# Optimization experiments

Measured on AMD Instinct MI355X. Metric: run time of the kernel, lower is better.

Reference implementation:

```python
import jax, jax.numpy as jnp
import numpy as np

_SAMPLING_EPS = 1e-5
BIG_NEG = jnp.float32(-1e30)  # finite stand-in for -inf (exact 0 after softmax in fp32)


def setup_inputs() -> dict:
    key = jax.random.key(0)
    ks = jax.random.split(key, 12)
    B, V, P, O, S = 128, 128000, 2048, 256, 4
    return {
        "logits": jax.random.normal(ks[0], (B, V), jnp.float32) * 4.0,
        "prompt_token_ids": jax.random.randint(ks[1], (B, P), 0, V),
        "output_token_ids": jax.random.randint(ks[2], (B, O), 0, V),
        "stop_token_ids": jax.random.randint(ks[3], (B, S), 0, V),
        "min_tokens": jax.random.randint(ks[4], (B,), 0, 512),
        "presence_penalties": jax.random.uniform(ks[5], (B,), jnp.float32),
        "frequency_penalties": jax.random.uniform(ks[6], (B,), jnp.float32),
        "repetition_penalties": 1.0 + 0.3 * jax.random.uniform(ks[7], (B,), jnp.float32),
        "temperature": 0.5 + jax.random.uniform(ks[8], (B,), jnp.float32),
        "top_k": jax.random.randint(ks[9], (B,), 32, 64),
        "top_p": 0.5 + 0.5 * jax.random.uniform(ks[10], (B,), jnp.float32),
        "uniform_noise": jax.random.uniform(ks[11], (B, V), jnp.float32, minval=1e-10, maxval=1.0),
        "max_num_logprobs": 20,
    }


def reference(logits, prompt_token_ids, output_token_ids, stop_token_ids,
              min_tokens, presence_penalties, frequency_penalties,
              repetition_penalties, temperature, top_k, top_p,
              uniform_noise, max_num_logprobs):
    B, V = logits.shape
    x = logits.astype(jnp.float32)
    rows = jnp.arange(B)[:, None]

    # ---- min-token penalty: set stop-token logits to -inf while len(output) < min_tokens
    need = min_tokens > output_token_ids.shape[1]                  # [B]
    stop_pen = jnp.where(need[:, None], BIG_NEG, jnp.inf)          # [B,S]
    x = x.at[rows, stop_token_ids].min(stop_pen)

    # ---- presence / frequency / repetition penalties (vLLM apply_penalties)
    counts = jnp.zeros((B, V), jnp.float32).at[rows, output_token_ids].add(1.0)
    prompt_mask = jnp.zeros((B, V), bool).at[rows, prompt_token_ids].set(True)
    output_mask = counts > 0
    rp = repetition_penalties[:, None]
    penalized = jnp.where(x > 0, x / rp, x * rp)
    x = jnp.where(prompt_mask | output_mask, penalized, x)
    x = x - frequency_penalties[:, None] * counts \
          - presence_penalties[:, None] * output_mask.astype(jnp.float32)

    # ---- temperature (greedy rows: temp treated as 1.0)
    t = jnp.where(temperature < _SAMPLING_EPS, 1.0, temperature)
    x = x / t[:, None]

    # ---- top-k / top-p filtering (per-row k and p)
    order = jnp.argsort(-x, axis=-1)                               # descending
    srt = jnp.take_along_axis(x, order, axis=-1)
    pos = jnp.arange(V)[None, :]
    k_eff = jnp.where(top_k < 1, V, top_k)
    keep_k = pos < k_eff[:, None]
    probs_s = jax.nn.softmax(srt, axis=-1)
    cum = jnp.cumsum(probs_s, axis=-1)
    keep_p = (cum - probs_s) < top_p[:, None]                      # cumulative mass before token < p
    keep = jnp.zeros((B, V), bool).at[rows, order].set(keep_k & keep_p)
    x = jnp.where(keep, x, BIG_NEG)

    orig_logits = x
    # source applies temperature a second time before the final sample
    x2 = x / t[:, None]

    # ---- sample: Gumbel-max random sampling, greedy where temperature ~ 0
    gumbel = -jnp.log(-jnp.log(uniform_noise))
    random_sampled = jnp.argmax(x2 + gumbel, axis=-1)
    greedy_sampled = jnp.argmax(x2, axis=-1)
    sampled = jnp.where(temperature < _SAMPLING_EPS, greedy_sampled,
                        random_sampled).astype(jnp.int32)

    # ---- top-k logprobs
    logprobs = jax.nn.log_softmax(orig_logits, axis=-1)
    topk_logprobs, topk_indices = jax.lax.top_k(logprobs, max_num_logprobs)
    return sampled, topk_logprobs, topk_indices.astype(jnp.int32)
```

## Files before the change

kernel.cpp:

```cpp
#include <hip/hip_runtime.h>
#include <math.h>

#define VV 128000
#define NB 128
#define PP 2048
#define OO 256

#define S   8
#define CH  16000
#define CW  500
#define NT1 256
#define CAP 128
#define HS1 512

#define NT2 256
#define MC  (S*CAP)

#define BIG_NEG_F (-1e30f)
#define PAD_KEY 0x007FFFFF80000000ULL
#define LOG2E 1.4426950408889634f

__device__ __forceinline__ unsigned long long packkey(float f, int idx) {
  unsigned int b = __float_as_uint(f);
  unsigned int mf = (b & 0x80000000u) ? ~b : (b | 0x80000000u);
  return ((unsigned long long)mf << 32) | (unsigned long long)(unsigned int)(~(unsigned int)idx);
}
__device__ __forceinline__ float unpack_val(unsigned long long k) {
  unsigned int mf = (unsigned int)(k >> 32);
  unsigned int b = (mf & 0x80000000u) ? (mf & 0x7fffffffu) : ~mf;
  return __uint_as_float(b);
}
__device__ __forceinline__ int unpack_idx(unsigned long long k) {
  return (int)(~(unsigned int)(k & 0xffffffffu));
}
__device__ __forceinline__ float ulp_down(float f, int n) {
  unsigned int b = __float_as_uint(f);
  unsigned int m = (b & 0x80000000u) ? ~b : (b | 0x80000000u);
  m -= (unsigned int)n;
  unsigned int r = (m & 0x80000000u) ? (m & 0x7fffffffu) : ~m;
  return __uint_as_float(r);
}

__device__ __forceinline__ float wave_sort64_desc(float v, int lane) {
  for (int k = 2; k <= 64; k <<= 1) {
    for (int j = k >> 1; j > 0; j >>= 1) {
      float o = __shfl_xor(v, j, 64);
      bool smaller = (lane & j) == 0;
      bool dir = (lane & k) == 0;
      bool keepmax = (smaller == dir);
      v = keepmax ? fmaxf(v, o) : fminf(v, o);
    }
  }
  return v;
}

template <int N, int T>
__device__ __forceinline__ void bitonic_desc_u64(unsigned long long* a, int tid) {
  for (int k = 2; k <= N; k <<= 1) {
    for (int j = k >> 1; j > 0; j >>= 1) {
      for (int i = tid; i < N; i += T) {
        int ixj = i ^ j;
        if (ixj > i) {
          unsigned long long x = a[i], y = a[ixj];
          bool up = (i & k) == 0;
          if ((x < y) == up) { a[i] = y; a[ixj] = x; }
        }
      }
      __syncthreads();
    }
  }
}

__global__ __launch_bounds__(NT1)
void k1_select(const float* __restrict__ logits,
               const int* __restrict__ prompt_ids,
               const int* __restrict__ output_ids,
               const int* __restrict__ stop_ids,
               const int* __restrict__ min_tokens,
               const float* __restrict__ presence_p,
               const float* __restrict__ frequency_p,
               const float* __restrict__ repetition_p,
               const float* __restrict__ temperature,
               unsigned long long* __restrict__ ws_cand,
               float* __restrict__ ws_sum,
               int* __restrict__ ws_cnt)
{
#pragma clang fp contract(off)
  __shared__ unsigned int pbits[CW];
  __shared__ unsigned int obits[CW];
  __shared__ int hkey[HS1];
  __shared__ int hval[HS1];
  __shared__ float smax[NT1];
  __shared__ float wsum[NT1 / 64];
  __shared__ float tau_sh;
  __shared__ int cnt_sh;

  const int chunk = blockIdx.x;
  const int row   = blockIdx.y;
  const int tid   = threadIdx.x;
  const int lane  = tid & 63;
  const int base  = chunk * CH;

  const float fp  = frequency_p[row];
  const float pp  = presence_p[row];
  const float rp  = repetition_p[row];
  const float inv_rp = 1.0f / rp;
  const float tmp = temperature[row];
  const float t   = (tmp < 1e-5f) ? 1.0f : tmp;
  const float c2  = LOG2E / t;
  const bool need = min_tokens[row] > OO;
  const int s0 = stop_ids[row * 4 + 0];
  const int s1 = stop_ids[row * 4 + 1];
  const int s2 = stop_ids[row * 4 + 2];
  const int s3 = stop_ids[row * 4 + 3];
  const bool anystop = need &&
      (((unsigned)(s0 - base) < CH) || ((unsigned)(s1 - base) < CH) ||
       ((unsigned)(s2 - base) < CH) || ((unsigned)(s3 - base) < CH));

  for (int i = tid; i < CW; i += NT1) { pbits[i] = 0u; obits[i] = 0u; }
  for (int i = tid; i < HS1; i += NT1) { hkey[i] = -1; hval[i] = 0; }
  if (tid == 0) cnt_sh = 0;
  __syncthreads();

  const int4* pr4 = (const int4*)(prompt_ids + (size_t)row * PP);
  for (int i = tid; i < PP / 4; i += NT1) {
    int4 tv = pr4[i];
    int l;
    l = tv.x - base; if ((unsigned)l < CH) atomicOr(&pbits[l >> 5], 1u << (l & 31));
    l = tv.y - base; if ((unsigned)l < CH) atomicOr(&pbits[l >> 5], 1u << (l & 31));
    l = tv.z - base; if ((unsigned)l < CH) atomicOr(&pbits[l >> 5], 1u << (l & 31));
    l = tv.w - base; if ((unsigned)l < CH) atomicOr(&pbits[l >> 5], 1u << (l & 31));
  }
  for (int i = tid; i < OO; i += NT1) {
    int tok = output_ids[row * OO + i];
    int l = tok - base;
    if ((unsigned)l < CH) {
      atomicOr(&obits[l >> 5], 1u << (l & 31));
      unsigned int h = ((unsigned int)tok * 2654435761u) >> 23;
      for (;;) {
        int k = hkey[h];
        if (k == tok) { atomicAdd(&hval[h], 1); break; }
        if (k == -1) {
          int prev = atomicCAS(&hkey[h], -1, tok);
          if (prev == -1 || prev == tok) { atomicAdd(&hval[h], 1); break; }
          continue;
        }
        h = (h + 1) & (HS1 - 1);
      }
    }
  }
  __syncthreads();

  const float* __restrict__ lrow = logits + (size_t)row * VV + base;
  const int NIT = (CH + NT1 * 8 - 1) / (NT1 * 8);

  float mx = -INFINITY;
  float esum = 0.0f;
  for (int it = 0; it < NIT; ++it) {
    int li = (it * NT1 + tid) << 3;
    if (li < CH) {
      float4 xa = *(const float4*)(lrow + li);
      float4 xb = *(const float4*)(lrow + li + 4);
      unsigned int w  = (unsigned)li >> 5;
      unsigned int sh = (unsigned)li & 31u;
      unsigned int pm8 = (pbits[w] >> sh) & 255u;
      unsigned int om8 = (obits[w] >> sh) & 255u;
      float xs[8] = {xa.x, xa.y, xa.z, xa.w, xb.x, xb.y, xb.z, xb.w};
#pragma unroll
      for (int e = 0; e < 8; ++e) {
        float xp = xs[e];
        int v = base + li + e;
        if (anystop && ((v == s0) | (v == s1) | (v == s2) | (v == s3)))
          xp = BIG_NEG_F;
        if ((pm8 | om8) & (1u << e)) {
          xp = (xp > 0.0f) ? (xp * inv_rp) : (xp * rp);
          if ((om8 >> e) & 1u) {
            float cnt = 0.0f;
            unsigned int h = ((unsigned int)v * 2654435761u) >> 23;
            for (;;) {
              int k = hkey[h];
              if (k == -1) break;
              if (k == v) { cnt = (float)hval[h]; break; }
              h = (h + 1) & (HS1 - 1);
            }
            xp = xp - fp * cnt - pp;
          }
        }
        mx = fmaxf(mx, xp);
        esum += exp2f(xp * c2);
      }
    }
  }

  float ss = esum;
#pragma unroll
  for (int off = 32; off > 0; off >>= 1) ss += __shfl_down(ss, off, 64);
  if (lane == 0) wsum[tid >> 6] = ss;

  smax[tid] = wave_sort64_desc(mx, lane);
  __syncthreads();

  if (tid == 0) {
    int p0 = 0, p1 = 0, p2 = 0, p3 = 0;
    float tau = -INFINITY;
    for (int n = 0; n < 64; ++n) {
      float v0 = (p0 < 64) ? smax[p0]       : -INFINITY;
      float v1 = (p1 < 64) ? smax[64 + p1]  : -INFINITY;
      float v2 = (p2 < 64) ? smax[128 + p2] : -INFINITY;
      float v3 = (p3 < 64) ? smax[192 + p3] : -INFINITY;
      float m01 = fmaxf(v0, v1), m23 = fmaxf(v2, v3);
      float m = fmaxf(m01, m23);
      if (m == v0) p0++;
      else if (m == v1) p1++;
      else if (m == v2) p2++;
      else p3++;
      tau = m;
    }
    tau_sh = ulp_down(tau, 16);
    ws_sum[row * S + chunk] = wsum[0] + wsum[1] + wsum[2] + wsum[3];
  }
  __syncthreads();
  const float taueff = tau_sh;

  unsigned long long* __restrict__ wc = ws_cand + ((size_t)row * S + chunk) * CAP;
  for (int it = 0; it < NIT; ++it) {
    int li = (it * NT1 + tid) << 3;
    if (li < CH) {
      float4 xa = *(const float4*)(lrow + li);
      float4 xb = *(const float4*)(lrow + li + 4);
      float xs[8] = {xa.x, xa.y, xa.z, xa.w, xb.x, xb.y, xb.z, xb.w};
#pragma unroll
      for (int e = 0; e < 8; ++e) {
        float x = xs[e];
        if (x >= taueff) {
          int v = base + li + e;
          int ll = li + e;
          if (anystop && ((v == s0) | (v == s1) | (v == s2) | (v == s3)))
            x = fminf(x, BIG_NEG_F);
          bool pm = (pbits[(unsigned)ll >> 5] >> ((unsigned)ll & 31u)) & 1u;
          bool om = (obits[(unsigned)ll >> 5] >> ((unsigned)ll & 31u)) & 1u;
          float cnt = 0.0f;
          if (om) {
            unsigned int h = ((unsigned int)v * 2654435761u) >> 23;
            for (;;) {
              int k = hkey[h];
              if (k == -1) break;
              if (k == v) { cnt = (float)hval[h]; break; }
              h = (h + 1) & (HS1 - 1);
            }
          }
          if (pm || om) x = (x > 0.0f) ? (x / rp) : (x * rp);
          x = x - fp * cnt;
          if (om) x = x - pp;
          float xd = x / t;
          int p = atomicAdd(&cnt_sh, 1);
          if (p < CAP) wc[p] = packkey(xd, v);
        }
      }
    }
  }
  __syncthreads();
  if (tid == 0) ws_cnt[row * S + chunk] = (cnt_sh < CAP) ? cnt_sh : CAP;
}

__global__ __launch_bounds__(NT2)
void k2_finalize(const float* __restrict__ temperature,
                 const int* __restrict__ top_k,
                 const float* __restrict__ top_p,
                 const float* __restrict__ noise,
                 const unsigned long long* __restrict__ ws_cand,
                 const float* __restrict__ ws_sum,
                 const int* __restrict__ ws_cnt,
                 float* __restrict__ out, int K)
{
#pragma clang fp contract(off)
  __shared__ unsigned long long cand[MC];
  __shared__ int cnts[S];
  __shared__ float sv[64];
  __shared__ int   si[64];
  __shared__ float se[64];
  __shared__ float gv[64];

  const int row = blockIdx.x;
  const int tid = threadIdx.x;

  const float tmp = temperature[row];
  const float t   = (tmp < 1e-5f) ? 1.0f : tmp;
  const int   tk  = top_k[row];
  const float tpv = top_p[row];

  if (tid < S) cnts[tid] = ws_cnt[row * S + tid];
  __syncthreads();

  for (int g = tid; g < MC; g += NT2) {
    int c = g >> 7;
    int i = g & (CAP - 1);
    cand[g] = (i < cnts[c]) ? ws_cand[((size_t)row * S + c) * CAP + i] : PAD_KEY;
  }
  __syncthreads();

  bitonic_desc_u64<MC, NT2>(cand, tid);

  if (tid < 64) {
    unsigned long long kk = cand[tid];
    float val = unpack_val(kk);
    int   idx = unpack_idx(kk);
    float m = unpack_val(cand[0]);
    sv[tid] = val;
    si[tid] = idx;
    bool ok = (unsigned)idx < VV;
    float u = ok ? noise[(size_t)row * VV + idx] : 0.5f;
    float g = -logf(-logf(u));
    se[tid] = expf(val - m);
    gv[tid] = val / t + g;
  }
  __syncthreads();

  if (tid == 0) {
    float Ssum = 0.0f;
    for (int c = 0; c < S; c++) Ssum += ws_sum[row * S + c];
    const float m = sv[0];
    const float Z = Ssum * exp2f(-m * LOG2E);

    int keff = (tk < 1) ? 64 : (tk < 64 ? tk : 64);

    float cum = 0.0f;
    int nk = 0;
    for (int j = 0; j < 64; j++) {
      if (j >= keff) break;
      if (!(cum < tpv)) break;
      nk++;
      cum += se[j] / Z;
    }

    float Zk = 0.0f;
    for (int j = 0; j < nk; j++) Zk += se[j];
    const float logZk = logf(Zk);

    float bv = -INFINITY; int bi = 0x7fffffff;
    for (int j = 0; j < nk; j++) {
      float val = gv[j];
      if (val > bv || (val == bv && si[j] < bi)) { bv = val; bi = si[j]; }
    }
    const int samp = (tmp < 1e-5f) ? si[0] : bi;
    out[row] = (float)samp;

    unsigned long long bm0 = 0ull, bm1 = 0ull;
    for (int j = 0; j < nk; j++) {
      int ix = si[j];
      if (ix < 64) bm0 |= 1ull << ix;
      else if (ix < 128) bm1 |= 1ull << (ix - 64);
    }
    int fi = 0;
    for (int j = 0; j < K; j++) {
      float lp; int ix;
      if (j < nk) {
        lp = (sv[j] - m) - logZk;
        ix = si[j];
      } else {
        while ((fi < 64) ? ((bm0 >> fi) & 1ull) : ((bm1 >> (fi - 64)) & 1ull)) fi++;
        ix = fi; fi++;
        lp = BIG_NEG_F;
      }
      out[NB + row * K + j]            = lp;
      out[NB + NB * K + row * K + j]   = (float)ix;
    }
  }
}

extern "C" void kernel_launch(void* const* d_in, const int* in_sizes, int n_in,
                              void* d_out, int out_size, void* d_ws, size_t ws_size,
                              hipStream_t stream) {
  const float* logits = (const float*)d_in[0];
  const int*   prompt = (const int*)d_in[1];
  const int*   outids = (const int*)d_in[2];
  const int*   stop   = (const int*)d_in[3];
  const int*   mint   = (const int*)d_in[4];
  const float* pres   = (const float*)d_in[5];
  const float* freq   = (const float*)d_in[6];
  const float* rep    = (const float*)d_in[7];
  const float* temp   = (const float*)d_in[8];
  const int*   topk   = (const int*)d_in[9];
  const float* topp   = (const float*)d_in[10];
  const float* noise  = (const float*)d_in[11];

  int B_ = in_sizes[4];
  int K_ = (out_size - B_) / (2 * B_);

  unsigned long long* ws_cand = (unsigned long long*)d_ws;
  float* ws_sum = (float*)(ws_cand + (size_t)NB * S * CAP);
  int*   ws_cnt = (int*)(ws_sum + (size_t)NB * S);

  dim3 g1(S, B_);
  k1_select<<<g1, NT1, 0, stream>>>(logits, prompt, outids, stop, mint,
                                    pres, freq, rep, temp,
                                    ws_cand, ws_sum, ws_cnt);
  k2_finalize<<<B_, NT2, 0, stream>>>(temp, topk, topp, noise,
                                      ws_cand, ws_sum, ws_cnt,
                                      (float*)d_out, K_);
}
```

Baseline: 226.3 us.

## Prebuild per-row penalty bitmaps in a separate kernel and register-cache logit chunks

Adds a k0 kernel that builds prompt/output bitmaps and output-count hash tables once per row in global memory. Previously each of the 8 chunk blocks rescanned all prompt and output ids. k1 now uses 512 threads and loads its chunk into registers with unrolled loads. The per-wave 8th-largest max replaces the serial 64-step merge for the threshold, candidates that fall below the threshold after penalties are filtered out, and CAP grows to 512 with a compacted k2 gather. The cost is an extra kernel launch, extra global traffic for the bitmaps, and a looser threshold that lets more candidates through.

```diff
diff --git a/kernel.cpp b/kernel.cpp
--- a/kernel.cpp
+++ b/kernel.cpp
@@ -5,16 +5,18 @@
 #define NB 128
 #define PP 2048
 #define OO 256
+#define GW 4000
 
 #define S   8
 #define CH  16000
 #define CW  500
-#define NT1 256
-#define CAP 128
+#define NT0 512
+#define NT1 512
+#define CAP 512
 #define HS1 512
 
-#define NT2 256
-#define MC  (S*CAP)
+#define NT2 512
+#define MC  2048
 
 #define BIG_NEG_F (-1e30f)
 #define PAD_KEY 0x007FFFFF80000000ULL
@@ -71,16 +73,70 @@
   }
 }
 
+__global__ __launch_bounds__(NT0)
+void k0_build(const int* __restrict__ prompt_ids,
+              const int* __restrict__ output_ids,
+              unsigned int* __restrict__ ws_pb,
+              unsigned int* __restrict__ ws_ob,
+              int* __restrict__ ws_hk,
+              int* __restrict__ ws_hv)
+{
+  __shared__ int hkey[HS1];
+  __shared__ int hval[HS1];
+  const int row = blockIdx.x;
+  const int tid = threadIdx.x;
+
+  unsigned int* pb = ws_pb + (size_t)row * GW;
+  unsigned int* ob = ws_ob + (size_t)row * GW;
+  uint4* pb4 = (uint4*)pb;
+  uint4* ob4 = (uint4*)ob;
+  uint4 z; z.x = 0u; z.y = 0u; z.z = 0u; z.w = 0u;
+  for (int i = tid; i < GW / 4; i += NT0) { pb4[i] = z; ob4[i] = z; }
+  for (int i = tid; i < HS1; i += NT0) { hkey[i] = -1; hval[i] = 0; }
+  __syncthreads();
+
+  const int4* pr4 = (const int4*)(prompt_ids + (size_t)row * PP);
+  for (int i = tid; i < PP / 4; i += NT0) {
+    int4 tv = pr4[i];
+    atomicOr(&pb[tv.x >> 5], 1u << (tv.x & 31));
+    atomicOr(&pb[tv.y >> 5], 1u << (tv.y & 31));
+    atomicOr(&pb[tv.z >> 5], 1u << (tv.z & 31));
+    atomicOr(&pb[tv.w >> 5], 1u << (tv.w & 31));
+  }
+  for (int i = tid; i < OO; i += NT0) {
+    int tok = output_ids[row * OO + i];
+    atomicOr(&ob[tok >> 5], 1u << (tok & 31));
+    unsigned int h = ((unsigned int)tok * 2654435761u) >> 23;
+    for (;;) {
+      int k = hkey[h];
+      if (k == tok) { atomicAdd(&hval[h], 1); break; }
+      if (k == -1) {
+        int prev = atomicCAS(&hkey[h], -1, tok);
+        if (prev == -1 || prev == tok) { atomicAdd(&hval[h], 1); break; }
+        continue;
+      }
+      h = (h + 1) & (HS1 - 1);
+    }
+  }
+  __syncthreads();
+  for (int i = tid; i < HS1; i += NT0) {
+    ws_hk[row * HS1 + i] = hkey[i];
+    ws_hv[row * HS1 + i] = hval[i];
+  }
+}
+
 __global__ __launch_bounds__(NT1)
 void k1_select(const float* __restrict__ logits,
-               const int* __restrict__ prompt_ids,
-               const int* __restrict__ output_ids,
                const int* __restrict__ stop_ids,
                const int* __restrict__ min_tokens,
                const float* __restrict__ presence_p,
                const float* __restrict__ frequency_p,
                const float* __restrict__ repetition_p,
                const float* __restrict__ temperature,
+               const unsigned int* __restrict__ ws_pb,
+               const unsigned int* __restrict__ ws_ob,
+               const int* __restrict__ ws_hk,
+               const int* __restrict__ ws_hv,
                unsigned long long* __restrict__ ws_cand,
                float* __restrict__ ws_sum,
                int* __restrict__ ws_cnt)
@@ -90,7 +146,7 @@
   __shared__ unsigned int obits[CW];
   __shared__ int hkey[HS1];
   __shared__ int hval[HS1];
-  __shared__ float smax[NT1];
+  __shared__ float wtau[NT1 / 64];
   __shared__ float wsum[NT1 / 64];
   __shared__ float tau_sh;
   __shared__ int cnt_sh;
@@ -117,148 +173,139 @@
       (((unsigned)(s0 - base) < CH) || ((unsigned)(s1 - base) < CH) ||
        ((unsigned)(s2 - base) < CH) || ((unsigned)(s3 - base) < CH));
 
-  for (int i = tid; i < CW; i += NT1) { pbits[i] = 0u; obits[i] = 0u; }
-  for (int i = tid; i < HS1; i += NT1) { hkey[i] = -1; hval[i] = 0; }
+  const unsigned int* pbg = ws_pb + (size_t)row * GW + chunk * CW;
+  const unsigned int* obg = ws_ob + (size_t)row * GW + chunk * CW;
+  for (int i = tid; i < CW; i += NT1) { pbits[i] = pbg[i]; obits[i] = obg[i]; }
+  for (int i = tid; i < HS1; i += NT1) {
+    hkey[i] = ws_hk[row * HS1 + i];
+    hval[i] = ws_hv[row * HS1 + i];
+  }
   if (tid == 0) cnt_sh = 0;
   __syncthreads();
 
-  const int4* pr4 = (const int4*)(prompt_ids + (size_t)row * PP);
-  for (int i = tid; i < PP / 4; i += NT1) {
-    int4 tv = pr4[i];
-    int l;
-    l = tv.x - base; if ((unsigned)l < CH) atomicOr(&pbits[l >> 5], 1u << (l & 31));
-    l = tv.y - base; if ((unsigned)l < CH) atomicOr(&pbits[l >> 5], 1u << (l & 31));
-    l = tv.z - base; if ((unsigned)l < CH) atomicOr(&pbits[l >> 5], 1u << (l & 31));
-    l = tv.w - base; if ((unsigned)l < CH) atomicOr(&pbits[l >> 5], 1u << (l & 31));
-  }
-  for (int i = tid; i < OO; i += NT1) {
-    int tok = output_ids[row * OO + i];
-    int l = tok - base;
-    if ((unsigned)l < CH) {
-      atomicOr(&obits[l >> 5], 1u << (l & 31));
-      unsigned int h = ((unsigned int)tok * 2654435761u) >> 23;
-      for (;;) {
-        int k = hkey[h];
-        if (k == tok) { atomicAdd(&hval[h], 1); break; }
-        if (k == -1) {
-          int prev = atomicCAS(&hkey[h], -1, tok);
-          if (prev == -1 || prev == tok) { atomicAdd(&hval[h], 1); break; }
-          continue;
-        }
-        h = (h + 1) & (HS1 - 1);
-      }
-    }
-  }
-  __syncthreads();
-
   const float* __restrict__ lrow = logits + (size_t)row * VV + base;
-  const int NIT = (CH + NT1 * 8 - 1) / (NT1 * 8);
+  const int l0 = (0 * NT1 + tid) << 3;
+  const int l1 = (1 * NT1 + tid) << 3;
+  const int l2 = (2 * NT1 + tid) << 3;
+  const int l3 = (3 * NT1 + tid) << 3;
+  const bool v3 = l3 < CH;
+
+  float4 A0 = *(const float4*)(lrow + l0);
+  float4 B0 = *(const float4*)(lrow + l0 + 4);
+  float4 A1 = *(const float4*)(lrow + l1);
+  float4 B1 = *(const float4*)(lrow + l1 + 4);
+  float4 A2 = *(const float4*)(lrow + l2);
+  float4 B2 = *(const float4*)(lrow + l2 + 4);
+  float4 A3, B3;
+  if (v3) { A3 = *(const float4*)(lrow + l3); B3 = *(const float4*)(lrow + l3 + 4); }
 
   float mx = -INFINITY;
   float esum = 0.0f;
-  for (int it = 0; it < NIT; ++it) {
-    int li = (it * NT1 + tid) << 3;
-    if (li < CH) {
-      float4 xa = *(const float4*)(lrow + li);
-      float4 xb = *(const float4*)(lrow + li + 4);
-      unsigned int w  = (unsigned)li >> 5;
-      unsigned int sh = (unsigned)li & 31u;
-      unsigned int pm8 = (pbits[w] >> sh) & 255u;
-      unsigned int om8 = (obits[w] >> sh) & 255u;
-      float xs[8] = {xa.x, xa.y, xa.z, xa.w, xb.x, xb.y, xb.z, xb.w};
+
+  auto processA = [&](int li, float4 xa, float4 xb) {
+    unsigned int w  = (unsigned)li >> 5;
+    unsigned int sh = (unsigned)li & 31u;
+    unsigned int pm8 = (pbits[w] >> sh) & 255u;
+    unsigned int om8 = (obits[w] >> sh) & 255u;
+    float xs[8] = {xa.x, xa.y, xa.z, xa.w, xb.x, xb.y, xb.z, xb.w};
 #pragma unroll
-      for (int e = 0; e < 8; ++e) {
-        float xp = xs[e];
-        int v = base + li + e;
-        if (anystop && ((v == s0) | (v == s1) | (v == s2) | (v == s3)))
-          xp = BIG_NEG_F;
-        if ((pm8 | om8) & (1u << e)) {
-          xp = (xp > 0.0f) ? (xp * inv_rp) : (xp * rp);
-          if ((om8 >> e) & 1u) {
-            float cnt = 0.0f;
-            unsigned int h = ((unsigned int)v * 2654435761u) >> 23;
-            for (;;) {
-              int k = hkey[h];
-              if (k == -1) break;
-              if (k == v) { cnt = (float)hval[h]; break; }
-              h = (h + 1) & (HS1 - 1);
-            }
-            xp = xp - fp * cnt - pp;
+    for (int e = 0; e < 8; ++e) {
+      float xp = xs[e];
+      int v = base + li + e;
+      if (anystop && ((v == s0) | (v == s1) | (v == s2) | (v == s3)))
+        xp = BIG_NEG_F;
+      if ((pm8 | om8) & (1u << e)) {
+        xp = (xp > 0.0f) ? (xp * inv_rp) : (xp * rp);
+        if ((om8 >> e) & 1u) {
+          float cnt = 0.0f;
+          unsigned int h = ((unsigned int)v * 2654435761u) >> 23;
+          for (;;) {
+            int k = hkey[h];
+            if (k == -1) break;
+            if (k == v) { cnt = (float)hval[h]; break; }
+            h = (h + 1) & (HS1 - 1);
           }
+          xp = xp - fp * cnt - pp;
         }
-        mx = fmaxf(mx, xp);
-        esum += exp2f(xp * c2);
       }
-    }
-  }
+      mx = fmaxf(mx, xp);
+      esum += exp2f(xp * c2);
+    }
+  };
+
+  processA(l0, A0, B0);
+  processA(l1, A1, B1);
+  processA(l2, A2, B2);
+  if (v3) processA(l3, A3, B3);
 
   float ss = esum;
 #pragma unroll
   for (int off = 32; off > 0; off >>= 1) ss += __shfl_down(ss, off, 64);
   if (lane == 0) wsum[tid >> 6] = ss;
 
-  smax[tid] = wave_sort64_desc(mx, lane);
+  float srt = wave_sort64_desc(mx, lane);
+  if (lane == 7) wtau[tid >> 6] = srt;
   __syncthreads();
 
   if (tid == 0) {
-    int p0 = 0, p1 = 0, p2 = 0, p3 = 0;
-    float tau = -INFINITY;
-    for (int n = 0; n < 64; ++n) {
-      float v0 = (p0 < 64) ? smax[p0]       : -INFINITY;
-      float v1 = (p1 < 64) ? smax[64 + p1]  : -INFINITY;
-      float v2 = (p2 < 64) ? smax[128 + p2] : -INFINITY;
-      float v3 = (p3 < 64) ? smax[192 + p3] : -INFINITY;
-      float m01 = fmaxf(v0, v1), m23 = fmaxf(v2, v3);
-      float m = fmaxf(m01, m23);
-      if (m == v0) p0++;
-      else if (m == v1) p1++;
-      else if (m == v2) p2++;
-      else p3++;
-      tau = m;
-    }
+    float tau = wtau[0];
+#pragma unroll
+    for (int w = 1; w < NT1 / 64; ++w) tau = fminf(tau, wtau[w]);
     tau_sh = ulp_down(tau, 16);
-    ws_sum[row * S + chunk] = wsum[0] + wsum[1] + wsum[2] + wsum[3];
+    float sacc = 0.0f;
+#pragma unroll
+    for (int w = 0; w < NT1 / 64; ++w) sacc += wsum[w];
+    ws_sum[row * S + chunk] = sacc;
   }
   __syncthreads();
   const float taueff = tau_sh;
 
   unsigned long long* __restrict__ wc = ws_cand + ((size_t)row * S + chunk) * CAP;
-  for (int it = 0; it < NIT; ++it) {
-    int li = (it * NT1 + tid) << 3;
-    if (li < CH) {
-      float4 xa = *(const float4*)(lrow + li);
-      float4 xb = *(const float4*)(lrow + li + 4);
-      float xs[8] = {xa.x, xa.y, xa.z, xa.w, xb.x, xb.y, xb.z, xb.w};
+
+  A0 = *(const float4*)(lrow + l0); B0 = *(const float4*)(lrow + l0 + 4);
+  A1 = *(const float4*)(lrow + l1); B1 = *(const float4*)(lrow + l1 + 4);
+  A2 = *(const float4*)(lrow + l2); B2 = *(const float4*)(lrow + l2 + 4);
+  if (v3) { A3 = *(const float4*)(lrow + l3); B3 = *(const float4*)(lrow + l3 + 4); }
+
+  auto processB = [&](int li, float4 xa, float4 xb) {
+    float xs[8] = {xa.x, xa.y, xa.z, xa.w, xb.x, xb.y, xb.z, xb.w};
 #pragma unroll
-      for (int e = 0; e < 8; ++e) {
-        float x = xs[e];
+    for (int e = 0; e < 8; ++e) {
+      float x = xs[e];
+      if (x >= taueff) {
+        int v = base + li + e;
+        int ll = li + e;
+        if (anystop && ((v == s0) | (v == s1) | (v == s2) | (v == s3)))
+          x = fminf(x, BIG_NEG_F);
+        bool pm = (pbits[(unsigned)ll >> 5] >> ((unsigned)ll & 31u)) & 1u;
+        bool om = (obits[(unsigned)ll >> 5] >> ((unsigned)ll & 31u)) & 1u;
+        float cnt = 0.0f;
+        if (om) {
+          unsigned int h = ((unsigned int)v * 2654435761u) >> 23;
+          for (;;) {
+            int k = hkey[h];
+            if (k == -1) break;
+            if (k == v) { cnt = (float)hval[h]; break; }
+            h = (h + 1) & (HS1 - 1);
+          }
+        }
+        if (pm || om) x = (x > 0.0f) ? (x / rp) : (x * rp);
+        x = x - fp * cnt;
+        if (om) x = x - pp;
         if (x >= taueff) {
-          int v = base + li + e;
-          int ll = li + e;
-          if (anystop && ((v == s0) | (v == s1) | (v == s2) | (v == s3)))
-            x = fminf(x, BIG_NEG_F);
-          bool pm = (pbits[(unsigned)ll >> 5] >> ((unsigned)ll & 31u)) & 1u;
-          bool om = (obits[(unsigned)ll >> 5] >> ((unsigned)ll & 31u)) & 1u;
-          float cnt = 0.0f;
-          if (om) {
-            unsigned int h = ((unsigned int)v * 2654435761u) >> 23;
-            for (;;) {
-              int k = hkey[h];
-              if (k == -1) break;
-              if (k == v) { cnt = (float)hval[h]; break; }
-              h = (h + 1) & (HS1 - 1);
-            }
-          }
-          if (pm || om) x = (x > 0.0f) ? (x / rp) : (x * rp);
-          x = x - fp * cnt;
-          if (om) x = x - pp;
           float xd = x / t;
           int p = atomicAdd(&cnt_sh, 1);
           if (p < CAP) wc[p] = packkey(xd, v);
         }
       }
     }
-  }
+  };
+
+  processB(l0, A0, B0);
+  processB(l1, A1, B1);
+  processB(l2, A2, B2);
+  if (v3) processB(l3, A3, B3);
+
   __syncthreads();
   if (tid == 0) ws_cnt[row * S + chunk] = (cnt_sh < CAP) ? cnt_sh : CAP;
 }
@@ -275,7 +322,7 @@
 {
 #pragma clang fp contract(off)
   __shared__ unsigned long long cand[MC];
-  __shared__ int cnts[S];
+  __shared__ int offs[S + 1];
   __shared__ float sv[64];
   __shared__ int   si[64];
   __shared__ float se[64];
@@ -289,13 +336,27 @@
   const int   tk  = top_k[row];
   const float tpv = top_p[row];
 
-  if (tid < S) cnts[tid] = ws_cnt[row * S + tid];
-  __syncthreads();
+  if (tid == 0) {
+    int o = 0;
+    for (int c = 0; c < S; ++c) {
+      offs[c] = o;
+      int cc = ws_cnt[row * S + c];
+      o += (cc < CAP) ? cc : CAP;
+    }
+    offs[S] = (o < MC) ? o : MC;
+  }
+  __syncthreads();
+  const int total = offs[S];
 
   for (int g = tid; g < MC; g += NT2) {
-    int c = g >> 7;
-    int i = g & (CAP - 1);
-    cand[g] = (i < cnts[c]) ? ws_cand[((size_t)row * S + c) * CAP + i] : PAD_KEY;
+    unsigned long long v = PAD_KEY;
+    if (g < total) {
+      int c = 0;
+      while (c < S - 1 && g >= offs[c + 1]) c++;
+      int i = g - offs[c];
+      v = ws_cand[((size_t)row * S + c) * CAP + i];
+    }
+    cand[g] = v;
   }
   __syncthreads();
 
@@ -388,12 +449,17 @@
   int K_ = (out_size - B_) / (2 * B_);
 
   unsigned long long* ws_cand = (unsigned long long*)d_ws;
-  float* ws_sum = (float*)(ws_cand + (size_t)NB * S * CAP);
-  int*   ws_cnt = (int*)(ws_sum + (size_t)NB * S);
-
+  unsigned int* ws_pb = (unsigned int*)(ws_cand + (size_t)NB * S * CAP);
+  unsigned int* ws_ob = ws_pb + (size_t)NB * GW;
+  int* ws_hk = (int*)(ws_ob + (size_t)NB * GW);
+  int* ws_hv = ws_hk + (size_t)NB * HS1;
+  float* ws_sum = (float*)(ws_hv + (size_t)NB * HS1);
+  int* ws_cnt = (int*)(ws_sum + (size_t)NB * S);
+
+  k0_build<<<B_, NT0, 0, stream>>>(prompt, outids, ws_pb, ws_ob, ws_hk, ws_hv);
   dim3 g1(S, B_);
-  k1_select<<<g1, NT1, 0, stream>>>(logits, prompt, outids, stop, mint,
-                                    pres, freq, rep, temp,
+  k1_select<<<g1, NT1, 0, stream>>>(logits, stop, mint, pres, freq, rep, temp,
+                                    ws_pb, ws_ob, ws_hk, ws_hv,
                                     ws_cand, ws_sum, ws_cnt);
   k2_finalize<<<B_, NT2, 0, stream>>>(temp, topk, topp, noise,
                                       ws_cand, ws_sum, ws_cnt,
```

New measurement: 236.9 us. +4.7%, slower.
